# Kernel tuning notes

Hardware: AMD Instinct MI355X
Metric: run time of the kernel (lower is better)

## Reference

```python
import jax, jax.numpy as jnp
import numpy as np

N = 4096
IN_F = 256
HEADS = 8
OUT_F = 64  # per-head dim
NEG_BIG = -9e15


def setup_inputs() -> dict:
    key = jax.random.key(0)
    k1, k2, k3, k4 = jax.random.split(key, 4)
    x = jax.random.normal(k1, (N, IN_F), dtype=jnp.float32)
    adj = jax.random.randint(k2, (N, N), 0, 2, dtype=jnp.int32)
    # linear weight (no bias): torch Linear(in, heads*out) -> store as [in, heads*out]
    lim_w = float(np.sqrt(6.0 / (IN_F + HEADS * OUT_F)))
    W = jax.random.uniform(k3, (IN_F, HEADS * OUT_F), minval=-lim_w, maxval=lim_w, dtype=jnp.float32)
    # attn param [1, heads, 2*out], xavier_uniform
    lim_a = float(np.sqrt(6.0 / (HEADS + 2 * OUT_F)))
    attn = jax.random.uniform(k4, (1, HEADS, 2 * OUT_F), minval=-lim_a, maxval=lim_a, dtype=jnp.float32)
    return {"x": x, "adj": adj, "W": W, "attn": attn}


def reference(x, adj, W, attn):
    n = x.shape[0]
    H = attn.shape[1]
    D = attn.shape[2] // 2
    h = (x @ W).reshape(n, H, D)                       # [N, H, D]
    a_src = attn[0, :, :D]                             # [H, D]
    a_dst = attn[0, :, D:]                             # [H, D]
    # separable GAT score: e[i, j, h] = a_src.h_i + a_dst.h_j
    s_src = jnp.einsum('nhd,hd->nh', h, a_src)         # [N, H]
    s_dst = jnp.einsum('nhd,hd->nh', h, a_dst)         # [N, H]
    e = s_src[:, None, :] + s_dst[None, :, :]          # [N, N, H]
    e = jnp.where(adj[:, :, None] > 0, e, jnp.float32(NEG_BIG))
    attention = jax.nn.softmax(e, axis=1)              # softmax over neighbor dim j
    h_prime = jnp.einsum('ijh,jhd->ihd', attention, h)  # [N, H, D]
    return h_prime.reshape(n, H * D)
```

## Files before the change

kernel.cpp:

```cpp
#include <hip/hip_runtime.h>
#include <hip/hip_bf16.h>
#include <stdint.h>

typedef __attribute__((ext_vector_type(4))) float  f32x4;
typedef __attribute__((ext_vector_type(8))) short  s16x8;
typedef __attribute__((ext_vector_type(4))) int    i32x4;
typedef __attribute__((ext_vector_type(8))) unsigned short u16x8;

#define NN 4096
#define GT_LD 4096
#define GT_ROWS 576
#define NUM_STRIDE (4096 * 512)

__device__ __forceinline__ unsigned short f2bf(float f) {
  uint32_t u = __builtin_bit_cast(uint32_t, f);
  u += 0x7FFF + ((u >> 16) & 1);
  return (unsigned short)(u >> 16);
}

__device__ __forceinline__ void gload_lds16(const void* g, void* l) {
  __builtin_amdgcn_global_load_lds(
      (const __attribute__((address_space(1))) unsigned int*)g,
      (__attribute__((address_space(3))) unsigned int*)l, 16, 0, 0);
}

__global__ __launch_bounds__(512) void k_small(const float* __restrict__ x,
                                               const float* __restrict__ W,
                                               unsigned short* __restrict__ xb,
                                               unsigned short* __restrict__ wt) {
  int bid = blockIdx.x;
  if (bid < 512) {
    int t = bid * 512 + threadIdx.x;
    f32x4 v = ((const f32x4*)x)[t];
    uint64_t r = (uint64_t)f2bf(v.x) | ((uint64_t)f2bf(v.y) << 16) |
                 ((uint64_t)f2bf(v.z) << 32) | ((uint64_t)f2bf(v.w) << 48);
    ((uint64_t*)xb)[t] = r;
  } else {
    int t = (bid - 512) * 512 + threadIdx.x;
    int c = t >> 8, k = t & 255;
    wt[t] = f2bf(W[k * 512 + c]);
  }
}

__global__ __launch_bounds__(512) void k_fat(const int* __restrict__ adj,
                                             unsigned short* __restrict__ ab,
                                             const unsigned short* __restrict__ xb,
                                             const unsigned short* __restrict__ wt,
                                             const float* __restrict__ attn,
                                             unsigned short* __restrict__ gt) {
  __shared__ unsigned short lx[16 * 256];
  __shared__ unsigned short lw[512 * 64];

  if (blockIdx.x >= 256) {
    int t = (blockIdx.x - 256) * 512 + threadIdx.x;
    const i32x4* p = (const i32x4*)adj;
    i32x4 v0 = p[2 * t], v1 = p[2 * t + 1];
    u16x8 r;
    r[0] = v0.x ? 0x3F80 : 0; r[1] = v0.y ? 0x3F80 : 0;
    r[2] = v0.z ? 0x3F80 : 0; r[3] = v0.w ? 0x3F80 : 0;
    r[4] = v1.x ? 0x3F80 : 0; r[5] = v1.y ? 0x3F80 : 0;
    r[6] = v1.z ? 0x3F80 : 0; r[7] = v1.w ? 0x3F80 : 0;
    ((u16x8*)ab)[t] = r;
    return;
  }

  const int tid = threadIdx.x;
  const int lane = tid & 63;
  const int h = tid >> 6;
  const int l15 = lane & 15, lg = lane >> 4;
  const int j0 = blockIdx.x * 16;

  {
    int L = tid * 16;
    int row = L >> 9, b = L & 511;
    int sb = b ^ ((row & 7) << 4);
    gload_lds16((const char*)xb + (j0 + row) * 512 + sb, (char*)lx + L);
  }

  f32x4 acc[4] = {};
  for (int kc = 0; kc < 4; ++kc) {
#pragma unroll
    for (int i = 0; i < 8; ++i) {
      int L = (i * 512 + tid) * 16;
      int c = L >> 7, b = L & 127;
      int sb = b ^ ((c & 7) << 4);
      gload_lds16((const char*)wt + c * 512 + kc * 128 + sb, (char*)lw + L);
    }
    asm volatile("s_waitcnt vmcnt(0)");
    __syncthreads();
#pragma unroll
    for (int kk = 0; kk < 2; ++kk) {
      int kby = kk * 64 + lg * 16;
      s16x8 a = *(const s16x8*)((const char*)lx + l15 * 512 +
                                ((kc * 128 + kby) ^ ((l15 & 7) << 4)));
#pragma unroll
      for (int n = 0; n < 4; ++n) {
        int c = h * 64 + n * 16 + l15;
        s16x8 b = *(const s16x8*)((const char*)lw + c * 128 + (kby ^ ((c & 7) << 4)));
        acc[n] = __builtin_amdgcn_mfma_f32_16x16x32_bf16(a, b, acc[n], 0, 0, 0);
      }
    }
    __syncthreads();
  }

  float adv[4];
#pragma unroll
  for (int n = 0; n < 4; ++n) adv[n] = attn[h * 128 + 64 + n * 16 + l15];
#pragma unroll
  for (int r = 0; r < 4; ++r) {
    float p = acc[0][r] * adv[0] + acc[1][r] * adv[1] +
              acc[2][r] * adv[2] + acc[3][r] * adv[3];
#pragma unroll
    for (int m = 1; m < 16; m <<= 1) p += __shfl_xor(p, m);
    float w = expf(p);
    int node = j0 + lg * 4 + r;
#pragma unroll
    for (int n = 0; n < 4; ++n) {
      int c = h * 64 + n * 16 + l15;
      gt[c * GT_LD + node] = f2bf(acc[n][r] * w);
    }
    if (l15 == 0) gt[(512 + h) * GT_LD + node] = f2bf(w);
  }
}

__global__ __launch_bounds__(256) void k_gemm(const unsigned short* __restrict__ A,
                                              const unsigned short* __restrict__ GT,
                                              float* __restrict__ out,
                                              float* __restrict__ numx,
                                              float* __restrict__ den,
                                              int klen) {
  __shared__ unsigned short lA[2][128 * 64];
  __shared__ unsigned short lB[2][64 * 64];
  const int tid = threadIdx.x;
  const int lane = tid & 63, wid = tid >> 6;
  const int wr = wid >> 1, wc = wid & 1;
  const int l15 = lane & 15, lg = lane >> 4;

  int g = blockIdx.x;
  int swz = (g & 7) * 36 + (g >> 3);
  int bx = swz / 9, by = swz % 9;
  const int row0 = bx * 128, c0 = by * 64;

  const int s = blockIdx.y;
  float* num = (s == 0) ? out : (numx + (s - 1) * NUM_STRIDE);
  float* dens = den + s * (4096 * 8);

  const char* Abase = (const char*)A + row0 * 8192 + s * klen * 2;
  const char* Bbase = (const char*)GT + c0 * 8192 + s * klen * 2;

  auto stageA = [&](unsigned short* dst, int kt) {
#pragma unroll
    for (int i = 0; i < 4; ++i) {
      int L = (i * 256 + tid) * 16;
      int r = L >> 7, b = L & 127;
      int sb = b ^ ((r & 7) << 4);
      gload_lds16(Abase + r * 8192 + kt * 128 + sb, (char*)dst + L);
    }
  };
  auto stageB = [&](unsigned short* dst, int kt) {
#pragma unroll
    for (int i = 0; i < 2; ++i) {
      int L = (i * 256 + tid) * 16;
      int r = L >> 7, b = L & 127;
      int sb = b ^ ((r & 7) << 4);
      gload_lds16(Bbase + r * 8192 + kt * 128 + sb, (char*)dst + L);
    }
  };

  f32x4 acc[4][2] = {};
  const int NKT = klen >> 6;

  stageA(lA[0], 0);
  stageB(lB[0], 0);
  asm volatile("s_waitcnt vmcnt(0)");
  __syncthreads();

  for (int kt = 0; kt < NKT; ++kt) {
    int cur = kt & 1;
    if (kt < NKT - 1) {
      stageA(lA[cur ^ 1], kt + 1);
      stageB(lB[cur ^ 1], kt + 1);
    }
#pragma unroll
    for (int kk = 0; kk < 2; ++kk) {
      int kby = kk * 64 + lg * 16;
      s16x8 a[4], b[2];
#pragma unroll
      for (int m = 0; m < 4; ++m) {
        int r = wr * 64 + m * 16 + l15;
        a[m] = *(const s16x8*)((const char*)lA[cur] + r * 128 + (kby ^ ((r & 7) << 4)));
      }
#pragma unroll
      for (int n = 0; n < 2; ++n) {
        int c = wc * 32 + n * 16 + l15;
        b[n] = *(const s16x8*)((const char*)lB[cur] + c * 128 + (kby ^ ((c & 7) << 4)));
      }
#pragma unroll
      for (int m = 0; m < 4; ++m)
#pragma unroll
        for (int n = 0; n < 2; ++n)
          acc[m][n] = __builtin_amdgcn_mfma_f32_16x16x32_bf16(a[m], b[n], acc[m][n], 0, 0, 0);
    }
    asm volatile("s_waitcnt vmcnt(0)");
    __syncthreads();
  }

#pragma unroll
  for (int m = 0; m < 4; ++m)
#pragma unroll
    for (int n = 0; n < 2; ++n) {
      int c = c0 + wc * 32 + n * 16 + l15;
#pragma unroll
      for (int r = 0; r < 4; ++r) {
        int i = row0 + wr * 64 + m * 16 + lg * 4 + r;
        float v = acc[m][n][r];
        if (c < 512) num[i * 512 + c] = v;
        else if (c < 520) dens[i * 8 + (c - 512)] = v;
      }
    }
}

__global__ __launch_bounds__(256) void k_final(float* __restrict__ out,
                                               const float* __restrict__ numx,
                                               const float* __restrict__ den,
                                               int S) {
  int t = blockIdx.x * 256 + threadIdx.x;
  int i = t >> 7, h = (t >> 4) & 7;
  f32x4 v = ((const f32x4*)out)[t];
  float d = den[i * 8 + h];
  for (int s = 1; s < S; ++s) {
    f32x4 u = ((const f32x4*)(numx + (s - 1) * NUM_STRIDE))[t];
    v.x += u.x; v.y += u.y; v.z += u.z; v.w += u.w;
    d += den[s * 4096 * 8 + i * 8 + h];
  }
  v.x /= d; v.y /= d; v.z /= d; v.w /= d;
  ((f32x4*)out)[t] = v;
}

extern "C" void kernel_launch(void* const* d_in, const int* in_sizes, int n_in,
                              void* d_out, int out_size, void* d_ws, size_t ws_size,
                              hipStream_t stream) {
  const float* x    = (const float*)d_in[0];
  const int*   adj  = (const int*)d_in[1];
  const float* W    = (const float*)d_in[2];
  const float* attn = (const float*)d_in[3];
  float* out = (float*)d_out;
  char* ws = (char*)d_ws;

  unsigned short* Ab  = (unsigned short*)(ws);
  unsigned short* GTp = (unsigned short*)(ws + 33554432);
  unsigned short* XB  = (unsigned short*)(ws + 38273024);
  unsigned short* WT  = (unsigned short*)(ws + 40370176);
  float*          DEN = (float*)(ws + 40632320);
  float*          NUMX = (float*)(ws + 41156608);

  int S = 1;
  if (ws_size >= 41156608ull + 3ull * NUM_STRIDE * 4 + 65536) S = 4;
  else if (ws_size >= 41156608ull + 1ull * NUM_STRIDE * 4 + 65536) S = 2;

  k_small<<<768, 512, 0, stream>>>(x, W, XB, WT);
  k_fat  <<<4352, 512, 0, stream>>>(adj, Ab, XB, WT, attn, GTp);
  dim3 ggrid(288, S);
  k_gemm <<<ggrid, 256, 0, stream>>>(Ab, GTp, out, NUMX, DEN, 4096 / S);
  k_final<<<2048, 256, 0, stream>>>(out, NUMX, DEN, S);
}
```

Baseline: 72.91 us.

## Fuse adjacency int-to-bf16 conversion into GEMM A-tile staging

Drops the separate pass that turned the int32 adjacency matrix into a bf16 buffer. The GEMM now loads int32 adj tiles into registers, converts them to bf16 0/1 with multiplies, and writes them swizzled into LDS, with the global load issued before the MFMA loop and the LDS write after it. This avoids writing and re-reading a 32MB intermediate, at the cost of more register pressure and reading int32 (twice the bytes) per A tile. The tile is read once per column block, so adj is re-read many times. Split-K is capped at 2 because the workspace shrinks.

Measured after the change: 70.81 us. 1.03x faster.

```diff
diff --git a/kernel.cpp b/kernel.cpp
--- a/kernel.cpp
+++ b/kernel.cpp
@@ -5,11 +5,10 @@
 typedef __attribute__((ext_vector_type(4))) float  f32x4;
 typedef __attribute__((ext_vector_type(8))) short  s16x8;
 typedef __attribute__((ext_vector_type(4))) int    i32x4;
-typedef __attribute__((ext_vector_type(8))) unsigned short u16x8;
+typedef __attribute__((ext_vector_type(4))) unsigned int u32x4;
 
 #define NN 4096
 #define GT_LD 4096
-#define GT_ROWS 576
 #define NUM_STRIDE (4096 * 512)
 
 __device__ __forceinline__ unsigned short f2bf(float f) {
@@ -42,28 +41,12 @@
   }
 }
 
-__global__ __launch_bounds__(512) void k_fat(const int* __restrict__ adj,
-                                             unsigned short* __restrict__ ab,
-                                             const unsigned short* __restrict__ xb,
+__global__ __launch_bounds__(512) void k_hgt(const unsigned short* __restrict__ xb,
                                              const unsigned short* __restrict__ wt,
                                              const float* __restrict__ attn,
                                              unsigned short* __restrict__ gt) {
   __shared__ unsigned short lx[16 * 256];
   __shared__ unsigned short lw[512 * 64];
-
-  if (blockIdx.x >= 256) {
-    int t = (blockIdx.x - 256) * 512 + threadIdx.x;
-    const i32x4* p = (const i32x4*)adj;
-    i32x4 v0 = p[2 * t], v1 = p[2 * t + 1];
-    u16x8 r;
-    r[0] = v0.x ? 0x3F80 : 0; r[1] = v0.y ? 0x3F80 : 0;
-    r[2] = v0.z ? 0x3F80 : 0; r[3] = v0.w ? 0x3F80 : 0;
-    r[4] = v1.x ? 0x3F80 : 0; r[5] = v1.y ? 0x3F80 : 0;
-    r[6] = v1.z ? 0x3F80 : 0; r[7] = v1.w ? 0x3F80 : 0;
-    ((u16x8*)ab)[t] = r;
-    return;
-  }
-
   const int tid = threadIdx.x;
   const int lane = tid & 63;
   const int h = tid >> 6;
@@ -123,7 +106,7 @@
   }
 }
 
-__global__ __launch_bounds__(256) void k_gemm(const unsigned short* __restrict__ A,
+__global__ __launch_bounds__(256) void k_gemm(const int* __restrict__ adj,
                                               const unsigned short* __restrict__ GT,
                                               float* __restrict__ out,
                                               float* __restrict__ numx,
@@ -145,16 +128,32 @@
   float* num = (s == 0) ? out : (numx + (s - 1) * NUM_STRIDE);
   float* dens = den + s * (4096 * 8);
 
-  const char* Abase = (const char*)A + row0 * 8192 + s * klen * 2;
-  const char* Bbase = (const char*)GT + c0 * 8192 + s * klen * 2;
-
-  auto stageA = [&](unsigned short* dst, int kt) {
+  const int rA = tid >> 3;
+  const int cA = (tid & 7) * 8;
+  const int* Ab0 = adj + (row0 + rA) * 4096 + s * klen + cA;
+  const int swzA = (cA * 2) ^ ((rA & 7) << 4);
+
+  const char* Bbase = (const char*)GT + c0 * 8192 + (long)s * klen * 2;
+
+  i32x4 p[8];
+  auto loadA = [&](int kt) {
+    const int* ap = Ab0 + kt * 64;
 #pragma unroll
     for (int i = 0; i < 4; ++i) {
-      int L = (i * 256 + tid) * 16;
-      int r = L >> 7, b = L & 127;
-      int sb = b ^ ((r & 7) << 4);
-      gload_lds16(Abase + r * 8192 + kt * 128 + sb, (char*)dst + L);
+      p[2 * i]     = *(const i32x4*)(ap + i * 32 * 4096);
+      p[2 * i + 1] = *(const i32x4*)(ap + i * 32 * 4096 + 4);
+    }
+  };
+  auto writeA = [&](unsigned short* dst) {
+#pragma unroll
+    for (int i = 0; i < 4; ++i) {
+      i32x4 a0 = p[2 * i], a1 = p[2 * i + 1];
+      u32x4 w;
+      w.x = (unsigned)a0.x * 0x3F80u + (unsigned)a0.y * 0x3F800000u;
+      w.y = (unsigned)a0.z * 0x3F80u + (unsigned)a0.w * 0x3F800000u;
+      w.z = (unsigned)a1.x * 0x3F80u + (unsigned)a1.y * 0x3F800000u;
+      w.w = (unsigned)a1.z * 0x3F80u + (unsigned)a1.w * 0x3F800000u;
+      *(u32x4*)((char*)dst + (i * 32 + rA) * 128 + swzA) = w;
     }
   };
   auto stageB = [&](unsigned short* dst, int kt) {
@@ -170,15 +169,16 @@
   f32x4 acc[4][2] = {};
   const int NKT = klen >> 6;
 
-  stageA(lA[0], 0);
+  loadA(0);
   stageB(lB[0], 0);
+  writeA(lA[0]);
   asm volatile("s_waitcnt vmcnt(0)");
   __syncthreads();
 
   for (int kt = 0; kt < NKT; ++kt) {
     int cur = kt & 1;
     if (kt < NKT - 1) {
-      stageA(lA[cur ^ 1], kt + 1);
+      loadA(kt + 1);
       stageB(lB[cur ^ 1], kt + 1);
     }
 #pragma unroll
@@ -201,6 +201,7 @@
         for (int n = 0; n < 2; ++n)
           acc[m][n] = __builtin_amdgcn_mfma_f32_16x16x32_bf16(a[m], b[n], acc[m][n], 0, 0, 0);
     }
+    if (kt < NKT - 1) writeA(lA[cur ^ 1]);
     asm volatile("s_waitcnt vmcnt(0)");
     __syncthreads();
   }
@@ -247,20 +248,18 @@
   float* out = (float*)d_out;
   char* ws = (char*)d_ws;
 
-  unsigned short* Ab  = (unsigned short*)(ws);
-  unsigned short* GTp = (unsigned short*)(ws + 33554432);
-  unsigned short* XB  = (unsigned short*)(ws + 38273024);
-  unsigned short* WT  = (unsigned short*)(ws + 40370176);
-  float*          DEN = (float*)(ws + 40632320);
-  float*          NUMX = (float*)(ws + 41156608);
+  unsigned short* GTp = (unsigned short*)(ws);
+  unsigned short* XB  = (unsigned short*)(ws + 4718592);
+  unsigned short* WT  = (unsigned short*)(ws + 6815744);
+  float*          DEN = (float*)(ws + 7077888);
+  float*          NUMX = (float*)(ws + 7602176);
 
   int S = 1;
-  if (ws_size >= 41156608ull + 3ull * NUM_STRIDE * 4 + 65536) S = 4;
-  else if (ws_size >= 41156608ull + 1ull * NUM_STRIDE * 4 + 65536) S = 2;
+  if (ws_size >= 7602176ull + 1ull * NUM_STRIDE * 4 + 65536) S = 2;
 
   k_small<<<768, 512, 0, stream>>>(x, W, XB, WT);
-  k_fat  <<<4352, 512, 0, stream>>>(adj, Ab, XB, WT, attn, GTp);
+  k_hgt  <<<256, 512, 0, stream>>>(XB, WT, attn, GTp);
   dim3 ggrid(288, S);
-  k_gemm <<<ggrid, 256, 0, stream>>>(Ab, GTp, out, NUMX, DEN, 4096 / S);
+  k_gemm <<<ggrid, 256, 0, stream>>>(adj, GTp, out, NUMX, DEN, 4096 / S);
   k_final<<<2048, 256, 0, stream>>>(out, NUMX, DEN, S);
 }
```

## Triple-buffer GEMM LDS staging with prefetch distance two and partial vmcnt waits

Applied to the files above, without the earlier changes.

The split-K GEMM moves from double to triple buffering in LDS. It prefetches two K-tiles ahead and waits with a partial vmcnt count, so the newest loads stay in flight instead of draining all outstanding loads each iteration. It also raises wave priority around the MFMA block and adds explicit barriers and lgkmcnt waits. The cost is 50% more LDS per block, which may lower occupancy, and a correctness dependence on the exact vmcnt counts matching the 6 loads issued per stage.

Result: slower. 84.39 us (+15.7%).

```diff
diff --git a/kernel.cpp b/kernel.cpp
--- a/kernel.cpp
+++ b/kernel.cpp
@@ -9,7 +9,6 @@
 
 #define NN 4096
 #define GT_LD 4096
-#define GT_ROWS 576
 #define NUM_STRIDE (4096 * 512)
 
 __device__ __forceinline__ unsigned short f2bf(float f) {
@@ -129,8 +128,8 @@
                                               float* __restrict__ numx,
                                               float* __restrict__ den,
                                               int klen) {
-  __shared__ unsigned short lA[2][128 * 64];
-  __shared__ unsigned short lB[2][64 * 64];
+  __shared__ unsigned short lA[3][128 * 64];
+  __shared__ unsigned short lB[3][64 * 64];
   const int tid = threadIdx.x;
   const int lane = tid & 63, wid = tid >> 6;
   const int wr = wid >> 1, wc = wid & 1;
@@ -145,8 +144,8 @@
   float* num = (s == 0) ? out : (numx + (s - 1) * NUM_STRIDE);
   float* dens = den + s * (4096 * 8);
 
-  const char* Abase = (const char*)A + row0 * 8192 + s * klen * 2;
-  const char* Bbase = (const char*)GT + c0 * 8192 + s * klen * 2;
+  const char* Abase = (const char*)A + row0 * 8192 + (long)s * klen * 2;
+  const char* Bbase = (const char*)GT + c0 * 8192 + (long)s * klen * 2;
 
   auto stageA = [&](unsigned short* dst, int kt) {
 #pragma unroll
@@ -170,17 +169,24 @@
   f32x4 acc[4][2] = {};
   const int NKT = klen >> 6;
 
-  stageA(lA[0], 0);
-  stageB(lB[0], 0);
-  asm volatile("s_waitcnt vmcnt(0)");
-  __syncthreads();
-
+  stageA(lA[0], 0); stageB(lB[0], 0);
+  stageA(lA[1], 1); stageB(lB[1], 1);
+
+  int cur = 0;
   for (int kt = 0; kt < NKT; ++kt) {
-    int cur = kt & 1;
-    if (kt < NKT - 1) {
-      stageA(lA[cur ^ 1], kt + 1);
-      stageB(lB[cur ^ 1], kt + 1);
-    }
+    int pf = cur + 2; if (pf >= 3) pf -= 3;
+    if (kt < NKT - 2) {
+      stageA(lA[pf], kt + 2);
+      stageB(lB[pf], kt + 2);
+      asm volatile("s_waitcnt vmcnt(12)" ::: "memory");
+    } else if (kt == NKT - 2) {
+      asm volatile("s_waitcnt vmcnt(6)" ::: "memory");
+    } else {
+      asm volatile("s_waitcnt vmcnt(0)" ::: "memory");
+    }
+    __builtin_amdgcn_s_barrier();
+
+    __builtin_amdgcn_s_setprio(1);
 #pragma unroll
     for (int kk = 0; kk < 2; ++kk) {
       int kby = kk * 64 + lg * 16;
@@ -201,8 +207,12 @@
         for (int n = 0; n < 2; ++n)
           acc[m][n] = __builtin_amdgcn_mfma_f32_16x16x32_bf16(a[m], b[n], acc[m][n], 0, 0, 0);
     }
-    asm volatile("s_waitcnt vmcnt(0)");
-    __syncthreads();
+    __builtin_amdgcn_s_setprio(0);
+
+    asm volatile("s_waitcnt lgkmcnt(0)" ::: "memory");
+    __builtin_amdgcn_sched_barrier(0);
+    __builtin_amdgcn_s_barrier();
+    cur = cur + 1; if (cur == 3) cur = 0;
   }
 
 #pragma unroll
```

## Drop GEMM LDS double buffering in favor of higher occupancy

Applied to the files above, without the earlier changes.

Replaces the double-buffered LDS staging in the split-K bf16 GEMM with a single buffer. Each k-tile is now loaded, synchronised, computed and synchronised again. This halves shared memory per block and adds a launch-bounds hint of 5 blocks per CU, so latency is meant to be hidden by more resident blocks rather than by in-block prefetch. The trade is that loads no longer overlap compute within a block. The explicit vmcnt wait before the barrier is also removed, which risks reading LDS before the async global-to-LDS loads land. Base offsets are widened to 64-bit.

Measured after the change: 66.98 us. 1.09x faster.

```diff
diff --git a/kernel.cpp b/kernel.cpp
--- a/kernel.cpp
+++ b/kernel.cpp
@@ -9,7 +9,6 @@
 
 #define NN 4096
 #define GT_LD 4096
-#define GT_ROWS 576
 #define NUM_STRIDE (4096 * 512)
 
 __device__ __forceinline__ unsigned short f2bf(float f) {
@@ -123,14 +122,14 @@
   }
 }
 
-__global__ __launch_bounds__(256) void k_gemm(const unsigned short* __restrict__ A,
-                                              const unsigned short* __restrict__ GT,
-                                              float* __restrict__ out,
-                                              float* __restrict__ numx,
-                                              float* __restrict__ den,
-                                              int klen) {
-  __shared__ unsigned short lA[2][128 * 64];
-  __shared__ unsigned short lB[2][64 * 64];
+__global__ __launch_bounds__(256, 5) void k_gemm(const unsigned short* __restrict__ A,
+                                                 const unsigned short* __restrict__ GT,
+                                                 float* __restrict__ out,
+                                                 float* __restrict__ numx,
+                                                 float* __restrict__ den,
+                                                 int klen) {
+  __shared__ unsigned short lA[128 * 64];
+  __shared__ unsigned short lB[64 * 64];
   const int tid = threadIdx.x;
   const int lane = tid & 63, wid = tid >> 6;
   const int wr = wid >> 1, wc = wid & 1;
@@ -145,42 +144,35 @@
   float* num = (s == 0) ? out : (numx + (s - 1) * NUM_STRIDE);
   float* dens = den + s * (4096 * 8);
 
-  const char* Abase = (const char*)A + row0 * 8192 + s * klen * 2;
-  const char* Bbase = (const char*)GT + c0 * 8192 + s * klen * 2;
-
-  auto stageA = [&](unsigned short* dst, int kt) {
+  const char* Abase = (const char*)A + row0 * 8192 + (long)s * klen * 2;
+  const char* Bbase = (const char*)GT + c0 * 8192 + (long)s * klen * 2;
+
+  auto stageA = [&](int kt) {
 #pragma unroll
     for (int i = 0; i < 4; ++i) {
       int L = (i * 256 + tid) * 16;
       int r = L >> 7, b = L & 127;
       int sb = b ^ ((r & 7) << 4);
-      gload_lds16(Abase + r * 8192 + kt * 128 + sb, (char*)dst + L);
+      gload_lds16(Abase + r * 8192 + kt * 128 + sb, (char*)lA + L);
     }
   };
-  auto stageB = [&](unsigned short* dst, int kt) {
+  auto stageB = [&](int kt) {
 #pragma unroll
     for (int i = 0; i < 2; ++i) {
       int L = (i * 256 + tid) * 16;
       int r = L >> 7, b = L & 127;
       int sb = b ^ ((r & 7) << 4);
-      gload_lds16(Bbase + r * 8192 + kt * 128 + sb, (char*)dst + L);
+      gload_lds16(Bbase + r * 8192 + kt * 128 + sb, (char*)lB + L);
     }
   };
 
   f32x4 acc[4][2] = {};
   const int NKT = klen >> 6;
 
-  stageA(lA[0], 0);
-  stageB(lB[0], 0);
-  asm volatile("s_waitcnt vmcnt(0)");
-  __syncthreads();
-
   for (int kt = 0; kt < NKT; ++kt) {
-    int cur = kt & 1;
-    if (kt < NKT - 1) {
-      stageA(lA[cur ^ 1], kt + 1);
-      stageB(lB[cur ^ 1], kt + 1);
-    }
+    stageA(kt);
+    stageB(kt);
+    __syncthreads();
 #pragma unroll
     for (int kk = 0; kk < 2; ++kk) {
       int kby = kk * 64 + lg * 16;
@@ -188,12 +180,12 @@
 #pragma unroll
       for (int m = 0; m < 4; ++m) {
         int r = wr * 64 + m * 16 + l15;
-        a[m] = *(const s16x8*)((const char*)lA[cur] + r * 128 + (kby ^ ((r & 7) << 4)));
+        a[m] = *(const s16x8*)((const char*)lA + r * 128 + (kby ^ ((r & 7) << 4)));
       }
 #pragma unroll
       for (int n = 0; n < 2; ++n) {
         int c = wc * 32 + n * 16 + l15;
-        b[n] = *(const s16x8*)((const char*)lB[cur] + c * 128 + (kby ^ ((c & 7) << 4)));
+        b[n] = *(const s16x8*)((const char*)lB + c * 128 + (kby ^ ((c & 7) << 4)));
       }
 #pragma unroll
       for (int m = 0; m < 4; ++m)
@@ -201,7 +193,6 @@
         for (int n = 0; n < 2; ++n)
           acc[m][n] = __builtin_amdgcn_mfma_f32_16x16x32_bf16(a[m], b[n], acc[m][n], 0, 0, 0);
     }
-    asm volatile("s_waitcnt vmcnt(0)");
     __syncthreads();
   }
 
```
